# Performance work log

Measured on AMD Instinct MI355X. Metric: run time of the kernel, lower is better.

Reference implementation:

```python
import jax, jax.numpy as jnp
import numpy as np
import math

EPS = 1e-5


def _layernorm(x, gamma, beta):
    mu = jnp.mean(x, axis=-1, keepdims=True)
    var = jnp.var(x, axis=-1, keepdims=True)
    return (x - mu) * jax.lax.rsqrt(var + EPS) * gamma + beta


def _quantum_head(x, theta_rx):
    # RX(x_i) then RX(theta_i) on wire i == RX(x_i + theta_i); product state,
    # CNOT ring is a Z-basis permutation => <Z_j> = prod_{i in S_j} cos(a_i)
    # with S_j = {0..j} for j>=1 (chain of CNOT(i,i+1)) and S_0 = {1..7}
    # (final CNOT(7,0) makes b0 = b1^...^b7).
    c = jnp.cos(x + theta_rx)                       # (B,S,8)
    cp = jnp.cumprod(c, axis=-1)                    # prefix products c0..cj
    z0 = jnp.prod(c[..., 1:], axis=-1, keepdims=True)
    return jnp.concatenate([z0, cp[..., 1:]], axis=-1)  # (B,S,8)


def _quantum_ffn(x, theta_ry):
    # RX(x_i) |0>, then RY(theta_i), measure Z: <Z_i> = cos(theta_i) * cos(x_i)
    return jnp.cos(theta_ry) * jnp.cos(x)


def setup_inputs() -> dict:
    key = jax.random.key(0)
    ks = jax.random.split(key, 6)
    B, S, E, F = 16, 2048, 8, 512
    return {
        'x': jax.random.normal(ks[0], (B, S, E), jnp.float32),
        'theta_rx': jax.random.normal(ks[1], (E,), jnp.float32),
        'w_out': jax.random.normal(ks[2], (E, E), jnp.float32) / math.sqrt(E),
        'theta_ry': jax.random.normal(ks[3], (E,), jnp.float32),
        'w1': jax.random.normal(ks[4], (F, E), jnp.float32) / math.sqrt(E),
        'b1': jnp.zeros((F,), jnp.float32),
        'w2': jax.random.normal(ks[5], (E, F), jnp.float32) / math.sqrt(F),
        'b2': jnp.zeros((E,), jnp.float32),
        'gamma1': jnp.ones((E,), jnp.float32),
        'beta1': jnp.zeros((E,), jnp.float32),
        'gamma2': jnp.ones((E,), jnp.float32),
        'beta2': jnp.zeros((E,), jnp.float32),
    }


def reference(x, theta_rx, w_out, theta_ry, w1, b1, w2, b2,
              gamma1, beta1, gamma2, beta2):
    B, S, E = x.shape
    H = 2
    D = E // H
    # --- quantum multi-head attention (shared head => q == k == v) ---
    z = _quantum_head(x, theta_rx)                       # (B,S,E)
    qh = z.reshape(B, S, H, D).transpose(0, 2, 1, 3)     # (B,H,S,D)
    scores = jnp.einsum('bhqd,bhkd->bhqk', qh, qh) / math.sqrt(D)
    attn = jax.nn.softmax(scores, axis=-1)
    out = jnp.einsum('bhqk,bhkd->bhqd', attn, qh)        # (B,H,S,D)
    out = out.transpose(0, 2, 1, 3).reshape(B, S, E)
    attn_out = out @ w_out.T                             # out_proj, no bias
    x1 = _layernorm(x + attn_out, gamma1, beta1)
    # --- quantum feed-forward ---
    zf = _quantum_ffn(x1, theta_ry)                      # (B,S,E)
    h = zf @ w1.T + b1                                   # (B,S,F)
    ffn_out = jax.nn.relu(h) @ w2.T + b2                 # (B,S,E)
    return _layernorm(x1 + ffn_out, gamma2, beta2)
```

## Files before the change

kernel.cpp:

```cpp
#include <hip/hip_runtime.h>
#include <math.h>
#include <utility>

#define NB 16
#define NS 2048
#define NE 8
#define NH 2
#define NF 512
#define DEG 6
#define NMONO 210
#define KPB 64
#define NCHUNK 32
#define PHI_LD 66
#define QPB 128
#define LNEPS 1e-5f
#define PART_STRIDE (5 * NMONO)

typedef float f32x2 __attribute__((ext_vector_type(2)));
typedef _Float16 h2 __attribute__((ext_vector_type(2)));

#if defined(__has_builtin)
# if __has_builtin(__builtin_amdgcn_fdot2)
#  define FDOT2(a,b,c) __builtin_amdgcn_fdot2((a),(b),(c),false)
# endif
#endif
#ifndef FDOT2
static __device__ __forceinline__ float fdot2_sw(h2 a, h2 b, float c) {
    return c + (float)a.x * (float)b.x + (float)a.y * (float)b.y;
}
# define FDOT2(a,b,c) fdot2_sw((a),(b),(c))
#endif

constexpr float ACOEF_C[7] = {0.99994459f, 2.00308514f, 2.00174650f,
                              1.30890404f, 0.65803033f, 0.31441604f, 0.10241921f};

constexpr int mono_e(int idx) {
    int i = 0;
    for (int e0 = 0; e0 <= DEG; ++e0)
        for (int e1 = 0; e1 <= DEG - e0; ++e1)
            for (int e2 = 0; e2 <= DEG - e0 - e1; ++e2)
                for (int e3 = 0; e3 <= DEG - e0 - e1 - e2; ++e3) {
                    if (i == idx) return (e0 << 12) | (e1 << 8) | (e2 << 4) | e3;
                    ++i;
                }
    return 0;
}
constexpr float mfact(int n) { float r = 1.f; for (int i = 2; i <= n; ++i) r *= (float)i; return r; }
constexpr float mono_c(int idx) {
    const int E = mono_e(idx);
    const int e0 = E >> 12, e1 = (E >> 8) & 15, e2 = (E >> 4) & 15, e3 = E & 15;
    const int d = e0 + e1 + e2 + e3;
    return ACOEF_C[d] * (mfact(d) / (mfact(e0) * mfact(e1) * mfact(e2) * mfact(e3)));
}

template <int BEG, class F, int... Is>
__device__ __forceinline__ void sf_impl(F f, std::integer_sequence<int, Is...>) {
    (f(std::integral_constant<int, BEG + Is>{}), ...);
}
template <int BEG, int END, class F>
__device__ __forceinline__ void static_for(F f) {
    sf_impl<BEG>(f, std::make_integer_sequence<int, END - BEG>{});
}

template <int BEG, int END>
__device__ __forceinline__ void phi_body(_Float16* __restrict__ Phi, int lane,
                                         const float (&pw0)[7], const float (&pw1)[7],
                                         const float (&pw2)[7], const float (&pw3)[7]) {
    static_for<BEG, END>([&](auto Ic) {
        constexpr int idx = Ic.value;
        constexpr int E = mono_e(idx);
        constexpr float C = mono_c(idx);
        const float v = C * (pw0[E >> 12] * pw1[(E >> 8) & 15]) *
                            (pw2[(E >> 4) & 15] * pw3[E & 15]);
        Phi[idx * PHI_LD + lane] = (_Float16)v;
    });
}

__global__ __launch_bounds__(256, 4)
void k1_moments(const float* __restrict__ x, const float* __restrict__ theta_rx,
                float* __restrict__ ws) {
    __shared__ _Float16 Phi[NMONO * PHI_LD];
    __shared__ _Float16 kvh[KPB / 2][8];
    __shared__ float th_s[8];

    const int t = threadIdx.x, bid = blockIdx.x;
    const int kc = bid & 31, h = (bid >> 5) & 1, b = bid >> 6;

    if (t < 8) th_s[t] = theta_rx[t];
    __syncthreads();

    const int lane = t & 63, wq = t >> 6;
    {
        const float* xr = x + ((size_t)b * NS + kc * KPB + lane) * NE;
        const float4 v0 = *reinterpret_cast<const float4*>(xr);
        const float4 v1 = *reinterpret_cast<const float4*>(xr + 4);
        const float c0 = __cosf(v0.x + th_s[0]), c1 = __cosf(v0.y + th_s[1]);
        const float c2 = __cosf(v0.z + th_s[2]), c3 = __cosf(v0.w + th_s[3]);
        const float c4 = __cosf(v1.x + th_s[4]), c5 = __cosf(v1.y + th_s[5]);
        const float c6 = __cosf(v1.z + th_s[6]), c7 = __cosf(v1.w + th_s[7]);
        const float p1 = c0*c1, p2 = p1*c2, p3 = p2*c3, p4 = p3*c4;
        const float p5 = p4*c5, p6 = p5*c6, p7 = p6*c7;
        float k0, k1v, k2v, k3v;
        if (h == 0) {
            const float s6 = c7*c6, s5 = s6*c5, s4 = s5*c4, s3 = s4*c3, s2 = s3*c2;
            k0 = s2*c1; k1v = p1; k2v = p2; k3v = p3;
        } else {
            k0 = p4; k1v = p5; k2v = p6; k3v = p7;
        }
        if (t < 64) {
            const int j = t >> 1, par = t & 1;
            kvh[j][0 + par] = (_Float16)k0;  kvh[j][2 + par] = (_Float16)k1v;
            kvh[j][4 + par] = (_Float16)k2v; kvh[j][6 + par] = (_Float16)k3v;
        }
        float pw0[7], pw1[7], pw2[7], pw3[7];
        pw0[0] = pw1[0] = pw2[0] = pw3[0] = 1.f;
        #pragma unroll
        for (int i = 1; i <= DEG; ++i) {
            pw0[i] = pw0[i-1] * k0;  pw1[i] = pw1[i-1] * k1v;
            pw2[i] = pw2[i-1] * k2v; pw3[i] = pw3[i-1] * k3v;
        }
        switch (wq) {
            case 0: phi_body<0,   53 >(Phi, lane, pw0, pw1, pw2, pw3); break;
            case 1: phi_body<53,  106>(Phi, lane, pw0, pw1, pw2, pw3); break;
            case 2: phi_body<106, 159>(Phi, lane, pw0, pw1, pw2, pw3); break;
            default: phi_body<159, 210>(Phi, lane, pw0, pw1, pw2, pw3); break;
        }
    }
    __syncthreads();

    if (t < NMONO) {
        const h2 one2 = {(_Float16)1.f, (_Float16)1.f};
        float a0 = 0.f, a1 = 0.f, a2 = 0.f, a3 = 0.f, a4 = 0.f;
        #pragma unroll 8
        for (int j = 0; j < KPB / 2; ++j) {
            const h2 phi2 = *reinterpret_cast<const h2*>(&Phi[t * PHI_LD + 2 * j]);
            const h2 kA = *reinterpret_cast<const h2*>(&kvh[j][0]);
            const h2 kB = *reinterpret_cast<const h2*>(&kvh[j][2]);
            const h2 kC = *reinterpret_cast<const h2*>(&kvh[j][4]);
            const h2 kD = *reinterpret_cast<const h2*>(&kvh[j][6]);
            a0 = FDOT2(phi2, kA, a0);
            a1 = FDOT2(phi2, kB, a1);
            a2 = FDOT2(phi2, kC, a2);
            a3 = FDOT2(phi2, kD, a3);
            a4 = FDOT2(phi2, one2, a4);
        }
        float* dst = ws + (size_t)bid * PART_STRIDE;
        dst[0 * NMONO + t] = a0;
        dst[1 * NMONO + t] = a1;
        dst[2 * NMONO + t] = a2;
        dst[3 * NMONO + t] = a3;
        dst[4 * NMONO + t] = a4;
    }
}

template <int BEG, int END>
__device__ __forceinline__ void p2_body(const float4* __restrict__ Mn,
                                        const float* __restrict__ Md, int base,
                                        const float (&pw0)[7], const float (&pw1)[7],
                                        const float (&pw2)[7], const float (&pw3)[7],
                                        f32x2& a01, f32x2& a23, float& ad) {
    static_for<BEG, END>([&](auto Ic) {
        constexpr int idx = Ic.value;
        constexpr int E = mono_e(idx);
        const float P = (pw0[E >> 12] * pw1[(E >> 8) & 15]) *
                        (pw2[(E >> 4) & 15] * pw3[E & 15]);
        const float4 mv = Mn[base + idx];
        const float  md = Md[base + idx];
        a01 += P * (f32x2){mv.x, mv.y};
        a23 += P * (f32x2){mv.z, mv.w};
        ad  += P * md;
    });
}

__global__ __launch_bounds__(1024)
void k2_main(const float* __restrict__ x, const float* __restrict__ theta_rx,
             const float* __restrict__ w_out, const float* __restrict__ theta_ry,
             const float* __restrict__ w1, const float* __restrict__ b1,
             const float* __restrict__ w2, const float* __restrict__ b2,
             const float* __restrict__ g1, const float* __restrict__ be1,
             const float* __restrict__ g2, const float* __restrict__ be2,
             const float* __restrict__ ws, float* __restrict__ out) {
    __shared__ float4 Mn_lds[2 * NMONO];
    __shared__ float  Md_lds[2 * NMONO];
    __shared__ float  z_c[8][QPB];
    __shared__ float  x1_c[8][QPB];
    __shared__ float  zf_c[8][QPB];
    __shared__ float  attn_c[8][QPB];
    __shared__ float  part_a[4][256][5];
    __shared__ float  part_f[8][8][QPB];
    __shared__ float  w1_s[NF][NE];
    __shared__ float  w2t_s[NF][NE];
    __shared__ float  b1_s[NF];
    __shared__ float  wout_s[NE][NE];
    __shared__ float  th_s[8], cry_s[8], g1_s[8], be1_s[8], g2_s[8], be2_s[8], b2_s[8];

    const int t = threadIdx.x, bid = blockIdx.x;
    const int b = bid >> 4, qc = bid & 15;

    if (t < 2 * NMONO) {
        const int h = (t >= NMONO) ? 1 : 0;
        const int a = t - h * NMONO;
        const float* src = ws + (size_t)((b * 2 + h) * NCHUNK) * PART_STRIDE;
        float s0 = 0.f, s1 = 0.f, s2 = 0.f, s3 = 0.f, s4 = 0.f;
        #pragma unroll 4
        for (int kc = 0; kc < NCHUNK; ++kc) {
            const float* p = src + (size_t)kc * PART_STRIDE;
            s0 += p[0 * NMONO + a]; s1 += p[1 * NMONO + a];
            s2 += p[2 * NMONO + a]; s3 += p[3 * NMONO + a];
            s4 += p[4 * NMONO + a];
        }
        Mn_lds[t] = make_float4(s0, s1, s2, s3);
        Md_lds[t] = s4;
    }

    for (int i = t; i < NF * NE; i += 1024) {
        ((float*)w1_s)[i] = w1[i];
        const int e = i >> 9, f = i & (NF - 1);
        w2t_s[f][e] = w2[i];
    }
    if (t < NF) b1_s[t] = b1[t];
    if (t < NE * NE) ((float*)wout_s)[t] = w_out[t];
    if (t < 8) {
        th_s[t]  = theta_rx[t];
        cry_s[t] = __cosf(theta_ry[t]);
        g1_s[t]  = g1[t];  be1_s[t] = be1[t];
        g2_s[t]  = g2[t];  be2_s[t] = be2[t];
        b2_s[t]  = b2[t];
    }
    __syncthreads();

    if (t < QPB) {
        const float* xr = x + ((size_t)b * NS + qc * QPB + t) * NE;
        const float4 v0 = *reinterpret_cast<const float4*>(xr);
        const float4 v1 = *reinterpret_cast<const float4*>(xr + 4);
        const float c0 = __cosf(v0.x + th_s[0]), c1 = __cosf(v0.y + th_s[1]);
        const float c2 = __cosf(v0.z + th_s[2]), c3 = __cosf(v0.w + th_s[3]);
        const float c4 = __cosf(v1.x + th_s[4]), c5 = __cosf(v1.y + th_s[5]);
        const float c6 = __cosf(v1.z + th_s[6]), c7 = __cosf(v1.w + th_s[7]);
        const float p1 = c0*c1, p2 = p1*c2, p3 = p2*c3, p4 = p3*c4;
        const float p5 = p4*c5, p6 = p5*c6, p7 = p6*c7;
        const float s6 = c7*c6, s5 = s6*c5, s4 = s5*c4, s3 = s4*c3, s2 = s3*c2;
        z_c[0][t] = s2*c1; z_c[1][t] = p1; z_c[2][t] = p2; z_c[3][t] = p3;
        z_c[4][t] = p4;    z_c[5][t] = p5; z_c[6][t] = p6; z_c[7][t] = p7;
    }
    __syncthreads();

    {
        const int g = t >> 8, u = t & 255, h = u >> 7, r = u & 127;
        const float u0 = z_c[h*4+0][r] * 0.25f, u1 = z_c[h*4+1][r] * 0.25f;
        const float u2 = z_c[h*4+2][r] * 0.25f, u3 = z_c[h*4+3][r] * 0.25f;
        float pw0[7], pw1[7], pw2[7], pw3[7];
        pw0[0] = pw1[0] = pw2[0] = pw3[0] = 1.f;
        #pragma unroll
        for (int i = 1; i <= DEG; ++i) {
            pw0[i] = pw0[i-1] * u0;  pw1[i] = pw1[i-1] * u1;
            pw2[i] = pw2[i-1] * u2;  pw3[i] = pw3[i-1] * u3;
        }
        f32x2 a01 = {0.f, 0.f}, a23 = {0.f, 0.f};
        float ad = 0.f;
        const int base = h * NMONO;
        switch (g) {
            case 0: p2_body<0,   53 >(Mn_lds, Md_lds, base, pw0, pw1, pw2, pw3, a01, a23, ad); break;
            case 1: p2_body<53,  106>(Mn_lds, Md_lds, base, pw0, pw1, pw2, pw3, a01, a23, ad); break;
            case 2: p2_body<106, 159>(Mn_lds, Md_lds, base, pw0, pw1, pw2, pw3, a01, a23, ad); break;
            default: p2_body<159, 210>(Mn_lds, Md_lds, base, pw0, pw1, pw2, pw3, a01, a23, ad); break;
        }
        float* pa = &part_a[g][u][0];
        pa[0] = a01.x; pa[1] = a01.y; pa[2] = a23.x; pa[3] = a23.y; pa[4] = ad;
    }
    __syncthreads();

    if (t < 256) {
        const int h = t >> 7, r = t & 127;
        float n0 = 0.f, n1 = 0.f, n2 = 0.f, n3 = 0.f, dd = 0.f;
        #pragma unroll
        for (int g = 0; g < 4; ++g) {
            const float* pa = &part_a[g][t][0];
            n0 += pa[0]; n1 += pa[1]; n2 += pa[2]; n3 += pa[3]; dd += pa[4];
        }
        const float inv = 1.0f / dd;
        attn_c[h*4+0][r] = n0 * inv; attn_c[h*4+1][r] = n1 * inv;
        attn_c[h*4+2][r] = n2 * inv; attn_c[h*4+3][r] = n3 * inv;
    }
    __syncthreads();

    if (t < QPB) {
        float av[NE];
        #pragma unroll
        for (int e = 0; e < NE; ++e) av[e] = attn_c[e][t];
        float y[NE];
        #pragma unroll
        for (int e = 0; e < NE; ++e) {
            float acc = 0.f;
            #pragma unroll
            for (int k = 0; k < NE; ++k) acc += av[k] * wout_s[e][k];
            y[e] = acc;
        }
        const float* xr = x + ((size_t)b * NS + qc * QPB + t) * NE;
        const float4 xv0 = *reinterpret_cast<const float4*>(xr);
        const float4 xv1 = *reinterpret_cast<const float4*>(xr + 4);
        float t1[NE];
        t1[0] = xv0.x + y[0]; t1[1] = xv0.y + y[1]; t1[2] = xv0.z + y[2]; t1[3] = xv0.w + y[3];
        t1[4] = xv1.x + y[4]; t1[5] = xv1.y + y[5]; t1[6] = xv1.z + y[6]; t1[7] = xv1.w + y[7];
        float mu = 0.f;
        #pragma unroll
        for (int e = 0; e < NE; ++e) mu += t1[e];
        mu *= 0.125f;
        float var = 0.f;
        #pragma unroll
        for (int e = 0; e < NE; ++e) { const float d = t1[e] - mu; var += d * d; }
        var *= 0.125f;
        const float inv1 = rsqrtf(var + LNEPS);
        #pragma unroll
        for (int e = 0; e < NE; ++e) {
            const float x1e = (t1[e] - mu) * inv1 * g1_s[e] + be1_s[e];
            x1_c[e][t] = x1e;
            zf_c[e][t] = cry_s[e] * __cosf(x1e);
        }
    }
    __syncthreads();

    {
        const int w = t >> 6, fs = w >> 1;
        const int row = (w & 1) * 64 + (t & 63);
        f32x2 zf01 = {zf_c[0][row], zf_c[1][row]};
        f32x2 zf23 = {zf_c[2][row], zf_c[3][row]};
        f32x2 zf45 = {zf_c[4][row], zf_c[5][row]};
        f32x2 zf67 = {zf_c[6][row], zf_c[7][row]};
        f32x2 acc01 = {0.f,0.f}, acc23 = {0.f,0.f}, acc45 = {0.f,0.f}, acc67 = {0.f,0.f};
        #pragma unroll 4
        for (int i = 0; i < 64; ++i) {
            const int f = fs * 64 + i;
            const float4 wa = *reinterpret_cast<const float4*>(&w1_s[f][0]);
            const float4 wb = *reinterpret_cast<const float4*>(&w1_s[f][4]);
            const f32x2 ha = zf01 * (f32x2){wa.x, wa.y} + zf23 * (f32x2){wa.z, wa.w};
            const f32x2 hb = zf45 * (f32x2){wb.x, wb.y} + zf67 * (f32x2){wb.z, wb.w};
            float hv = b1_s[f] + ha.x + ha.y + hb.x + hb.y;
            hv = fmaxf(hv, 0.f);
            const float4 ua = *reinterpret_cast<const float4*>(&w2t_s[f][0]);
            const float4 ub = *reinterpret_cast<const float4*>(&w2t_s[f][4]);
            acc01 += hv * (f32x2){ua.x, ua.y};
            acc23 += hv * (f32x2){ua.z, ua.w};
            acc45 += hv * (f32x2){ub.x, ub.y};
            acc67 += hv * (f32x2){ub.z, ub.w};
        }
        part_f[fs][0][row] = acc01.x; part_f[fs][1][row] = acc01.y;
        part_f[fs][2][row] = acc23.x; part_f[fs][3][row] = acc23.y;
        part_f[fs][4][row] = acc45.x; part_f[fs][5][row] = acc45.y;
        part_f[fs][6][row] = acc67.x; part_f[fs][7][row] = acc67.y;
    }
    __syncthreads();

    {
        const int e = t >> 7, r = t & 127;
        float s = 0.f;
        #pragma unroll
        for (int fs = 0; fs < 8; ++fs) s += part_f[fs][e][r];
        zf_c[e][r] = x1_c[e][r] + s + b2_s[e];
    }
    __syncthreads();

    if (t < QPB) {
        float t2[NE];
        #pragma unroll
        for (int e = 0; e < NE; ++e) t2[e] = zf_c[e][t];
        float mu = 0.f;
        #pragma unroll
        for (int e = 0; e < NE; ++e) mu += t2[e];
        mu *= 0.125f;
        float var = 0.f;
        #pragma unroll
        for (int e = 0; e < NE; ++e) { const float d = t2[e] - mu; var += d * d; }
        var *= 0.125f;
        const float inv2 = rsqrtf(var + LNEPS);
        float o[NE];
        #pragma unroll
        for (int e = 0; e < NE; ++e) o[e] = (t2[e] - mu) * inv2 * g2_s[e] + be2_s[e];
        float4* o4 = reinterpret_cast<float4*>(out + ((size_t)b * NS + qc * QPB + t) * NE);
        o4[0] = make_float4(o[0], o[1], o[2], o[3]);
        o4[1] = make_float4(o[4], o[5], o[6], o[7]);
    }
}

extern "C" void kernel_launch(void* const* d_in, const int* in_sizes, int n_in,
                              void* d_out, int out_size, void* d_ws, size_t ws_size,
                              hipStream_t stream) {
    const float* x        = (const float*)d_in[0];
    const float* theta_rx = (const float*)d_in[1];
    const float* w_out    = (const float*)d_in[2];
    const float* theta_ry = (const float*)d_in[3];
    const float* w1       = (const float*)d_in[4];
    const float* b1       = (const float*)d_in[5];
    const float* w2       = (const float*)d_in[6];
    const float* b2       = (const float*)d_in[7];
    const float* g1       = (const float*)d_in[8];
    const float* be1      = (const float*)d_in[9];
    const float* g2       = (const float*)d_in[10];
    const float* be2      = (const float*)d_in[11];
    float* out = (float*)d_out;
    float* ws  = (float*)d_ws;

    k1_moments<<<dim3(NB * NH * NCHUNK), dim3(256), 0, stream>>>(x, theta_rx, ws);
    k2_main<<<dim3(NB * (NS / QPB)), dim3(1024), 0, stream>>>(
        x, theta_rx, w_out, theta_ry, w1, b1, w2, b2, g1, be1, g2, be2, ws, out);
}
```

Before: 36.13 us.

## Register-block attention and FFN phases to reuse LDS weight loads across rows

In k2_main, the attention-moment phase now gives each thread two query rows using 512 threads instead of 1024, so each Mn/Md LDS load is shared across two rows. The FFN phase uses 256 threads with four rows each, so each w1/w2 LDS load is reused four times, and part_f is transposed and padded to stride 9. k1 now loads the kvh row as a single 16-byte vector. The aim is fewer LDS reads per FLOP, at the cost of more registers per thread and fewer active threads (less parallelism and latency hiding) in those phases.

```diff
diff --git a/kernel.cpp b/kernel.cpp
--- a/kernel.cpp
+++ b/kernel.cpp
@@ -80,7 +80,7 @@
 void k1_moments(const float* __restrict__ x, const float* __restrict__ theta_rx,
                 float* __restrict__ ws) {
     __shared__ _Float16 Phi[NMONO * PHI_LD];
-    __shared__ _Float16 kvh[KPB / 2][8];
+    __shared__ __align__(16) _Float16 kvh[KPB / 2][8];
     __shared__ float th_s[8];
 
     const int t = threadIdx.x, bid = blockIdx.x;
@@ -134,10 +134,11 @@
         #pragma unroll 8
         for (int j = 0; j < KPB / 2; ++j) {
             const h2 phi2 = *reinterpret_cast<const h2*>(&Phi[t * PHI_LD + 2 * j]);
-            const h2 kA = *reinterpret_cast<const h2*>(&kvh[j][0]);
-            const h2 kB = *reinterpret_cast<const h2*>(&kvh[j][2]);
-            const h2 kC = *reinterpret_cast<const h2*>(&kvh[j][4]);
-            const h2 kD = *reinterpret_cast<const h2*>(&kvh[j][6]);
+            const float4 kv4 = *reinterpret_cast<const float4*>(&kvh[j][0]);
+            const h2 kA = __builtin_bit_cast(h2, kv4.x);
+            const h2 kB = __builtin_bit_cast(h2, kv4.y);
+            const h2 kC = __builtin_bit_cast(h2, kv4.z);
+            const h2 kD = __builtin_bit_cast(h2, kv4.w);
             a0 = FDOT2(phi2, kA, a0);
             a1 = FDOT2(phi2, kB, a1);
             a2 = FDOT2(phi2, kC, a2);
@@ -154,21 +155,22 @@
 }
 
 template <int BEG, int END>
-__device__ __forceinline__ void p2_body(const float4* __restrict__ Mn,
-                                        const float* __restrict__ Md, int base,
-                                        const float (&pw0)[7], const float (&pw1)[7],
-                                        const float (&pw2)[7], const float (&pw3)[7],
-                                        f32x2& a01, f32x2& a23, float& ad) {
+__device__ __forceinline__ void p2_body2(const float4* __restrict__ Mn,
+                                         const float* __restrict__ Md, int base,
+                                         const float (&pwA)[4][7], const float (&pwB)[4][7],
+                                         f32x2& a01A, f32x2& a23A, float& adA,
+                                         f32x2& a01B, f32x2& a23B, float& adB) {
     static_for<BEG, END>([&](auto Ic) {
         constexpr int idx = Ic.value;
         constexpr int E = mono_e(idx);
-        const float P = (pw0[E >> 12] * pw1[(E >> 8) & 15]) *
-                        (pw2[(E >> 4) & 15] * pw3[E & 15]);
+        constexpr int e0 = E >> 12, e1 = (E >> 8) & 15, e2 = (E >> 4) & 15, e3 = E & 15;
         const float4 mv = Mn[base + idx];
         const float  md = Md[base + idx];
-        a01 += P * (f32x2){mv.x, mv.y};
-        a23 += P * (f32x2){mv.z, mv.w};
-        ad  += P * md;
+        const f32x2 m01 = {mv.x, mv.y}, m23 = {mv.z, mv.w};
+        const float PA = (pwA[0][e0] * pwA[1][e1]) * (pwA[2][e2] * pwA[3][e3]);
+        const float PB = (pwB[0][e0] * pwB[1][e1]) * (pwB[2][e2] * pwB[3][e3]);
+        a01A += PA * m01;  a23A += PA * m23;  adA += PA * md;
+        a01B += PB * m01;  a23B += PB * m23;  adB += PB * md;
     });
 }
 
@@ -187,7 +189,7 @@
     __shared__ float  zf_c[8][QPB];
     __shared__ float  attn_c[8][QPB];
     __shared__ float  part_a[4][256][5];
-    __shared__ float  part_f[8][8][QPB];
+    __shared__ float  part_f[8][QPB][9];
     __shared__ float  w1_s[NF][NE];
     __shared__ float  w2t_s[NF][NE];
     __shared__ float  b1_s[NF];
@@ -245,28 +247,35 @@
     }
     __syncthreads();
 
-    {
-        const int g = t >> 8, u = t & 255, h = u >> 7, r = u & 127;
-        const float u0 = z_c[h*4+0][r] * 0.25f, u1 = z_c[h*4+1][r] * 0.25f;
-        const float u2 = z_c[h*4+2][r] * 0.25f, u3 = z_c[h*4+3][r] * 0.25f;
-        float pw0[7], pw1[7], pw2[7], pw3[7];
-        pw0[0] = pw1[0] = pw2[0] = pw3[0] = 1.f;
-        #pragma unroll
-        for (int i = 1; i <= DEG; ++i) {
-            pw0[i] = pw0[i-1] * u0;  pw1[i] = pw1[i-1] * u1;
-            pw2[i] = pw2[i-1] * u2;  pw3[i] = pw3[i-1] * u3;
-        }
-        f32x2 a01 = {0.f, 0.f}, a23 = {0.f, 0.f};
-        float ad = 0.f;
+    if (t < 512) {
+        const int w = t >> 6, l = t & 63;
+        const int g = w >> 1, h = w & 1;
+        const int rA = l, rB = l + 64;
+        float pwA[4][7], pwB[4][7];
+        #pragma unroll
+        for (int d = 0; d < 4; ++d) {
+            const float uA = z_c[h*4+d][rA] * 0.25f;
+            const float uB = z_c[h*4+d][rB] * 0.25f;
+            pwA[d][0] = 1.f; pwB[d][0] = 1.f;
+            #pragma unroll
+            for (int i = 1; i <= DEG; ++i) {
+                pwA[d][i] = pwA[d][i-1] * uA;
+                pwB[d][i] = pwB[d][i-1] * uB;
+            }
+        }
+        f32x2 a01A = {0.f,0.f}, a23A = {0.f,0.f}, a01B = {0.f,0.f}, a23B = {0.f,0.f};
+        float adA = 0.f, adB = 0.f;
         const int base = h * NMONO;
         switch (g) {
-            case 0: p2_body<0,   53 >(Mn_lds, Md_lds, base, pw0, pw1, pw2, pw3, a01, a23, ad); break;
-            case 1: p2_body<53,  106>(Mn_lds, Md_lds, base, pw0, pw1, pw2, pw3, a01, a23, ad); break;
-            case 2: p2_body<106, 159>(Mn_lds, Md_lds, base, pw0, pw1, pw2, pw3, a01, a23, ad); break;
-            default: p2_body<159, 210>(Mn_lds, Md_lds, base, pw0, pw1, pw2, pw3, a01, a23, ad); break;
-        }
-        float* pa = &part_a[g][u][0];
-        pa[0] = a01.x; pa[1] = a01.y; pa[2] = a23.x; pa[3] = a23.y; pa[4] = ad;
+            case 0: p2_body2<0,   53 >(Mn_lds, Md_lds, base, pwA, pwB, a01A, a23A, adA, a01B, a23B, adB); break;
+            case 1: p2_body2<53,  106>(Mn_lds, Md_lds, base, pwA, pwB, a01A, a23A, adA, a01B, a23B, adB); break;
+            case 2: p2_body2<106, 159>(Mn_lds, Md_lds, base, pwA, pwB, a01A, a23A, adA, a01B, a23B, adB); break;
+            default: p2_body2<159, 210>(Mn_lds, Md_lds, base, pwA, pwB, a01A, a23A, adA, a01B, a23B, adB); break;
+        }
+        float* pa = &part_a[g][h * 128 + rA][0];
+        pa[0] = a01A.x; pa[1] = a01A.y; pa[2] = a23A.x; pa[3] = a23A.y; pa[4] = adA;
+        float* pb = &part_a[g][h * 128 + rB][0];
+        pb[0] = a01B.x; pb[1] = a01B.y; pb[2] = a23B.x; pb[3] = a23B.y; pb[4] = adB;
     }
     __syncthreads();
 
@@ -320,34 +329,48 @@
     }
     __syncthreads();
 
-    {
-        const int w = t >> 6, fs = w >> 1;
-        const int row = (w & 1) * 64 + (t & 63);
-        f32x2 zf01 = {zf_c[0][row], zf_c[1][row]};
-        f32x2 zf23 = {zf_c[2][row], zf_c[3][row]};
-        f32x2 zf45 = {zf_c[4][row], zf_c[5][row]};
-        f32x2 zf67 = {zf_c[6][row], zf_c[7][row]};
-        f32x2 acc01 = {0.f,0.f}, acc23 = {0.f,0.f}, acc45 = {0.f,0.f}, acc67 = {0.f,0.f};
+    if (t < 256) {
+        const int fs = t >> 5;
+        const int rr = t & 31;
+        f32x2 zf01[4], zf23[4], zf45[4], zf67[4];
+        #pragma unroll
+        for (int k = 0; k < 4; ++k) {
+            const int row = rr + 32 * k;
+            zf01[k] = (f32x2){zf_c[0][row], zf_c[1][row]};
+            zf23[k] = (f32x2){zf_c[2][row], zf_c[3][row]};
+            zf45[k] = (f32x2){zf_c[4][row], zf_c[5][row]};
+            zf67[k] = (f32x2){zf_c[6][row], zf_c[7][row]};
+        }
+        f32x2 a01[4] = {}, a23[4] = {}, a45[4] = {}, a67[4] = {};
         #pragma unroll 4
         for (int i = 0; i < 64; ++i) {
             const int f = fs * 64 + i;
             const float4 wa = *reinterpret_cast<const float4*>(&w1_s[f][0]);
             const float4 wb = *reinterpret_cast<const float4*>(&w1_s[f][4]);
-            const f32x2 ha = zf01 * (f32x2){wa.x, wa.y} + zf23 * (f32x2){wa.z, wa.w};
-            const f32x2 hb = zf45 * (f32x2){wb.x, wb.y} + zf67 * (f32x2){wb.z, wb.w};
-            float hv = b1_s[f] + ha.x + ha.y + hb.x + hb.y;
-            hv = fmaxf(hv, 0.f);
+            const float bb = b1_s[f];
             const float4 ua = *reinterpret_cast<const float4*>(&w2t_s[f][0]);
             const float4 ub = *reinterpret_cast<const float4*>(&w2t_s[f][4]);
-            acc01 += hv * (f32x2){ua.x, ua.y};
-            acc23 += hv * (f32x2){ua.z, ua.w};
-            acc45 += hv * (f32x2){ub.x, ub.y};
-            acc67 += hv * (f32x2){ub.z, ub.w};
-        }
-        part_f[fs][0][row] = acc01.x; part_f[fs][1][row] = acc01.y;
-        part_f[fs][2][row] = acc23.x; part_f[fs][3][row] = acc23.y;
-        part_f[fs][4][row] = acc45.x; part_f[fs][5][row] = acc45.y;
-        part_f[fs][6][row] = acc67.x; part_f[fs][7][row] = acc67.y;
+            const f32x2 wa01 = {wa.x, wa.y}, wa23 = {wa.z, wa.w};
+            const f32x2 wb45 = {wb.x, wb.y}, wb67 = {wb.z, wb.w};
+            const f32x2 ua01 = {ua.x, ua.y}, ua23 = {ua.z, ua.w};
+            const f32x2 ub45 = {ub.x, ub.y}, ub67 = {ub.z, ub.w};
+            #pragma unroll
+            for (int k = 0; k < 4; ++k) {
+                const f32x2 ha = zf01[k] * wa01 + zf23[k] * wa23;
+                const f32x2 hb = zf45[k] * wb45 + zf67[k] * wb67;
+                float hv = bb + ha.x + ha.y + hb.x + hb.y;
+                hv = fmaxf(hv, 0.f);
+                a01[k] += hv * ua01;  a23[k] += hv * ua23;
+                a45[k] += hv * ub45;  a67[k] += hv * ub67;
+            }
+        }
+        #pragma unroll
+        for (int k = 0; k < 4; ++k) {
+            const int row = rr + 32 * k;
+            float* pf = &part_f[fs][row][0];
+            pf[0] = a01[k].x; pf[1] = a01[k].y; pf[2] = a23[k].x; pf[3] = a23[k].y;
+            pf[4] = a45[k].x; pf[5] = a45[k].y; pf[6] = a67[k].x; pf[7] = a67[k].y;
+        }
     }
     __syncthreads();
 
@@ -355,7 +378,7 @@
         const int e = t >> 7, r = t & 127;
         float s = 0.f;
         #pragma unroll
-        for (int fs = 0; fs < 8; ++fs) s += part_f[fs][e][r];
+        for (int fs = 0; fs < 8; ++fs) s += part_f[fs][r][e];
         zf_c[e][r] = x1_c[e][r] + s + b2_s[e];
     }
     __syncthreads();
```

Result: no change. 35.60 us (-1.5%).
